# Performance work log

Measured on AMD Instinct MI355X. Metric: run time of the kernel, lower is better.

## Reference

```python
import jax, jax.numpy as jnp
import numpy as np

B, S, H, NH = 8, 512, 4096, 64
HD = H // NH  # head dim = 64
LN_EPS = 1e-12
TOL_BITS = 16


def quant16(x):
    """Per-tensor dynamic fixed-point quantization to 16 bits.

    int_bit_width = ceil(log2(max|x|)) + 1 (sign bit); frac = 16 - int_bits.
    Values are rounded to the fixed-point grid and clipped to int16 range.
    """
    m = jnp.max(jnp.abs(x))
    int_bw = jnp.ceil(jnp.log2(jnp.maximum(m, 1e-12))) + 1.0
    frac_bw = jnp.asarray(TOL_BITS, x.dtype) - int_bw
    scale = jnp.exp2(frac_bw).astype(x.dtype)
    q = jnp.clip(jnp.round(x * scale), -32768.0, 32767.0) / scale
    return q


def setup_inputs() -> dict:
    key = jax.random.key(0)
    ks = jax.random.split(key, 6)
    s = 0.02
    return {
        "input_ids": jax.random.normal(ks[0], (B, S, H), jnp.float32),
        "attention_mask": jnp.zeros((B, 1, 1, S), jnp.float32),
        "Wq": jax.random.normal(ks[1], (H, H), jnp.float32) * s,
        "bq": jnp.zeros((H,), jnp.float32),
        "Wk": jax.random.normal(ks[2], (H, H), jnp.float32) * s,
        "bk": jnp.zeros((H,), jnp.float32),
        "Wv": jax.random.normal(ks[3], (H, H), jnp.float32) * s,
        "bv": jnp.zeros((H,), jnp.float32),
        "Wd": jax.random.normal(ks[4], (H, H), jnp.float32) * s,
        "bd": jnp.zeros((H,), jnp.float32),
        "ln_w": jnp.ones((H,), jnp.float32),
        "ln_b": jnp.zeros((H,), jnp.float32),
    }


def reference(input_ids, attention_mask, Wq, bq, Wk, bk, Wv, bv, Wd, bd, ln_w, ln_b):
    x = input_ids  # [B,S,H]
    # Q/K/V projections (torch Linear: y = x @ W.T + b), each followed by quant
    q = quant16(jnp.einsum('bsh,oh->bso', x, Wq) + bq)
    k = quant16(jnp.einsum('bsh,oh->bso', x, Wk) + bk)
    v = quant16(jnp.einsum('bsh,oh->bso', x, Wv) + bv)
    # split heads -> [B,NH,S,HD]
    q = q.reshape(B, S, NH, HD).transpose(0, 2, 1, 3)
    k = k.reshape(B, S, NH, HD).transpose(0, 2, 1, 3)
    v = v.reshape(B, S, NH, HD).transpose(0, 2, 1, 3)
    scores = jnp.einsum('bnqd,bnkd->bnqk', q, k) / np.sqrt(HD).astype(np.float32)
    scores = quant16(scores)
    scores = scores + attention_mask
    probs = jax.nn.softmax(scores, axis=-1)
    probs = quant16(probs)
    ctx = quant16(jnp.einsum('bnqk,bnkd->bnqd', probs, v))
    ctx = ctx.transpose(0, 2, 1, 3)  # [B,S,NH,HD]
    # dense: w = Wd.T reshaped to (NH, HD, H)
    w = Wd.T.reshape(NH, HD, H)
    proj = quant16(jnp.einsum('bfnd,ndh->bfh', ctx, w) + bd)
    # residual + LayerNorm
    y = x + proj
    mu = jnp.mean(y, axis=-1, keepdims=True)
    var = jnp.mean(jnp.square(y - mu), axis=-1, keepdims=True)
    y = (y - mu) / jnp.sqrt(var + LN_EPS) * ln_w + ln_b
    return quant16(y)
```

## Files before the change

kernel.cpp:

```cpp
#include <hip/hip_runtime.h>
#include <hip/hip_bf16.h>
#include <stdint.h>


typedef __attribute__((ext_vector_type(4))) float f32x4;
typedef __attribute__((ext_vector_type(8))) __bf16 bf16x8;

__device__ inline unsigned short f2bf(float f) {
  union { float f; unsigned u; } c; c.f = f;
  unsigned r = (c.u + 0x7fffu + ((c.u >> 16) & 1u)) >> 16;
  return (unsigned short)r;
}

__device__ inline void gload_lds16(const void* g, void* l) {
  __builtin_amdgcn_global_load_lds(
      (const __attribute__((address_space(1))) void*)g,
      (__attribute__((address_space(3))) void*)l, 16, 0, 0);
}

__global__ __launch_bounds__(256) void conv_all(
    const float* __restrict__ x, const float* __restrict__ wq,
    const float* __restrict__ wk, const float* __restrict__ wv,
    const float* __restrict__ wd, unsigned short* __restrict__ out) {
  int i = blockIdx.x * 256 + threadIdx.x;
  int reg = i >> 21;
  int off = i & 2097151;
  const float* src = (reg == 0) ? x : (reg == 1) ? wq : (reg == 2) ? wk
                     : (reg == 3) ? wv : wd;
  const float4* ip = (const float4*)src;
  float4 a = ip[off * 2], b = ip[off * 2 + 1];
  union { unsigned short s[8]; uint4 v; } o;
  o.s[0] = f2bf(a.x); o.s[1] = f2bf(a.y); o.s[2] = f2bf(a.z); o.s[3] = f2bf(a.w);
  o.s[4] = f2bf(b.x); o.s[5] = f2bf(b.y); o.s[6] = f2bf(b.z); o.s[7] = f2bf(b.w);
  ((uint4*)out)[i] = o.v;
}

template <int BIAS_MODE, int OUT_BF16>
__global__ __launch_bounds__(512, 2) void gemm_8p(
    const unsigned short* __restrict__ A, const unsigned short* __restrict__ Bw,
    const float* __restrict__ bias0, const float* __restrict__ bias1,
    const float* __restrict__ bias2, void* __restrict__ Cout,
    int M, int N, int K) {
  extern __shared__ unsigned short lds[];
  const int nbm = M >> 8, nbn = N >> 8, nwg = nbm * nbn;
  const int bid = blockIdx.x;
  const int wg = (bid & 7) * (nwg >> 3) + (bid >> 3);
  const int bm = wg % nbm, bn = wg / nbm;
  const int tid = threadIdx.x, w = tid >> 6, l = tid & 63;
  const int wr = w >> 2, wc = w & 3;
  const int lr = l & 15, lg = l >> 4;
  const unsigned short* gA = A + (size_t)bm * 256 * K;
  const unsigned short* gB = Bw + (size_t)bn * 256 * K;
  const int NT = K >> 6;
  const int srow = tid >> 3;
  const int scol = ((tid & 7) ^ (srow & 7)) << 3;
  f32x4 acc[8][4] = {};
  bf16x8 a[8], b[8];

#define STG(op, buf, h, kt)                                                    \
  {                                                                            \
    const unsigned short* g_ = (op) ? gB : gA;                                 \
    _Pragma("unroll")                                                          \
    for (int j_ = 0; j_ < 2; ++j_) {                                           \
      gload_lds16(                                                             \
          g_ + (size_t)((h) * 128 + j_ * 64 + srow) * K + (kt) * 64 + scol,    \
          &lds[((op) * 2 + (buf)) * 16384 + ((h) * 128 + j_ * 64) * 64 +       \
               w * 512]);                                                      \
    }                                                                          \
  }

#define RDA(buf, m, kk)                                                        \
  (*(const bf16x8*)&lds[(buf) * 16384 + (wr * 128 + (m) * 16 + lr) * 64 +      \
                        ((((kk) * 4 + lg) ^ (lr & 7)) << 3)])
#define RDB(buf, n, kk)                                                        \
  (*(const bf16x8*)&lds[(2 + (buf)) * 16384 + (wc * 64 + (n) * 16 + lr) * 64 + \
                        ((((kk) * 4 + lg) ^ (lr & 7)) << 3)])

#define LDA(buf, mh)                                                           \
  _Pragma("unroll")                                                            \
  for (int m_ = 0; m_ < 4; ++m_) {                                             \
    a[m_ * 2 + 0] = RDA(buf, (mh) * 4 + m_, 0);                                \
    a[m_ * 2 + 1] = RDA(buf, (mh) * 4 + m_, 1);                                \
  }
#define LDB(buf, nh)                                                           \
  _Pragma("unroll")                                                            \
  for (int n_ = 0; n_ < 2; ++n_) {                                             \
    b[((nh) * 2 + n_) * 2 + 0] = RDB(buf, (nh) * 2 + n_, 0);                   \
    b[((nh) * 2 + n_) * 2 + 1] = RDB(buf, (nh) * 2 + n_, 1);                   \
  }

#define MM(mbase, nbase)                                                       \
  __builtin_amdgcn_s_setprio(1);                                               \
  _Pragma("unroll")                                                            \
  for (int m_ = 0; m_ < 4; ++m_) {                                             \
    _Pragma("unroll")                                                          \
    for (int n_ = 0; n_ < 2; ++n_) {                                           \
      acc[(mbase) + m_][(nbase) + n_] =                                        \
          __builtin_amdgcn_mfma_f32_16x16x32_bf16(                             \
              a[m_ * 2], b[((nbase) + n_) * 2], acc[(mbase) + m_][(nbase) + n_],\
              0, 0, 0);                                                        \
      acc[(mbase) + m_][(nbase) + n_] =                                        \
          __builtin_amdgcn_mfma_f32_16x16x32_bf16(                             \
              a[m_ * 2 + 1], b[((nbase) + n_) * 2 + 1],                        \
              acc[(mbase) + m_][(nbase) + n_], 0, 0, 0);                       \
    }                                                                          \
  }                                                                            \
  __builtin_amdgcn_s_setprio(0);

#define BAR() __builtin_amdgcn_s_barrier()
#define VMW(n) asm volatile("s_waitcnt vmcnt(" #n ")" ::: "memory")

  STG(0, 0, 0, 0); STG(0, 0, 1, 0); STG(1, 0, 0, 0); STG(1, 0, 1, 0);
  STG(0, 1, 0, 1);
  VMW(2);
  BAR();

  const int NI = NT >> 1;
  for (int i = 0; i < NI; ++i) {
    const int t1 = 2 * i + 1, t2 = 2 * i + 2, t3 = 2 * i + 3;
    const bool s2 = t2 < NT, s3 = t3 < NT;
    LDA(0, 0); LDB(0, 0);
    STG(0, 1, 1, t1);
    BAR(); MM(0, 0); BAR();
    LDB(0, 1);
    STG(1, 1, 0, t1);
    BAR(); MM(0, 2); BAR();
    LDA(0, 1);
    STG(1, 1, 1, t1);
    BAR(); MM(4, 2); BAR();
    if (s2) STG(0, 0, 0, t2);
    BAR(); MM(4, 0);
    if (s2) VMW(2); else VMW(0);
    BAR();
    LDA(1, 0); LDB(1, 0);
    if (s2) STG(0, 0, 1, t2);
    BAR(); MM(0, 0); BAR();
    LDB(1, 1);
    if (s2) STG(1, 0, 0, t2);
    BAR(); MM(0, 2); BAR();
    LDA(1, 1);
    if (s2) STG(1, 0, 1, t2);
    BAR(); MM(4, 2); BAR();
    if (s3) STG(0, 1, 0, t3);
    BAR(); MM(4, 0);
    if (s3) VMW(2); else VMW(0);
    BAR();
  }

#pragma unroll
  for (int n = 0; n < 4; ++n) {
    int col = bn * 256 + wc * 64 + n * 16 + lr;
    float bv = 0.f;
    if (BIAS_MODE == 1) bv = bias0[col];
    else if (BIAS_MODE == 2)
      bv = (col < 4096) ? bias0[col] : (col < 8192 ? bias1[col - 4096] : bias2[col - 8192]);
#pragma unroll
    for (int m = 0; m < 8; ++m) {
#pragma unroll
      for (int r = 0; r < 4; ++r) {
        int row = bm * 256 + wr * 128 + m * 16 + lg * 4 + r;
        float v = acc[m][n][r] + bv;
        if (OUT_BF16)
          ((unsigned short*)Cout)[(size_t)row * N + col] = f2bf(v);
        else
          ((float*)Cout)[(size_t)row * N + col] = v;
      }
    }
  }
#undef STG
#undef RDA
#undef RDB
#undef LDA
#undef LDB
#undef MM
#undef BAR
#undef VMW
}

__global__ __launch_bounds__(512) void attn_kernel(
    const unsigned short* __restrict__ qkv, const float* __restrict__ mask,
    unsigned short* __restrict__ ctx) {
  extern __shared__ char smem[];
  unsigned short* Kt = (unsigned short*)smem;
  unsigned short* Vt = Kt + 512 * 64;
  unsigned short* Pb = Vt + 64 * 512;
  float* Mb = (float*)(Pb + 8 * 16 * 64);

  const int bid = blockIdx.x;
  const int b = bid >> 6, h = bid & 63;
  const int tid = threadIdx.x, w = tid >> 6, l = tid & 63;
  const size_t tokbase = (size_t)b * 512;

  Mb[tid < 512 ? tid : 0] = mask[b * 512 + (tid < 512 ? tid : 0)];
#pragma unroll
  for (int it = 0; it < 8; ++it) {
    int idx = it * 512 + tid;
    int row = idx >> 3, g = (idx & 7) << 3;
    const unsigned short* src = qkv + (tokbase + row) * 12288 + 4096 + h * 64 + g;
    uint4 v = *(const uint4*)src;
    *(uint4*)&Kt[row * 64 + (g ^ ((row & 7) << 3))] = v;
  }
#pragma unroll
  for (int it = 0; it < 8; ++it) {
    int idx = it * 512 + tid;
    int key = idx >> 3, g = (idx & 7) << 3;
    const unsigned short* src = qkv + (tokbase + key) * 12288 + 8192 + h * 64 + g;
    uint4 v = *(const uint4*)src;
    const unsigned short* e = (const unsigned short*)&v;
#pragma unroll
    for (int i = 0; i < 8; i++) {
      int d = g + i;
      Vt[d * 512 + (key ^ ((d & 7) << 3))] = e[i];
    }
  }
  __syncthreads();

  unsigned short* Pw = Pb + w * 16 * 64;
  const int lr = l & 15, lg = l >> 4;

  for (int c = 0; c < 4; ++c) {
    int q0 = w * 64 + c * 16;
    const unsigned short* qsrc = qkv + (tokbase + q0 + lr) * 12288 + h * 64 + lg * 8;
    bf16x8 qa0 = *(const bf16x8*)qsrc;
    bf16x8 qa1 = *(const bf16x8*)(qsrc + 32);
    f32x4 sc[32];
    f32x4 zero = {0.f, 0.f, 0.f, 0.f};
#pragma unroll
    for (int n = 0; n < 32; n++) {
      int key = n * 16 + lr;
      bf16x8 kb0 = *(const bf16x8*)&Kt[key * 64 + ((lg * 8) ^ ((key & 7) << 3))];
      bf16x8 kb1 = *(const bf16x8*)&Kt[key * 64 + ((32 + lg * 8) ^ ((key & 7) << 3))];
      f32x4 a = __builtin_amdgcn_mfma_f32_16x16x32_bf16(qa0, kb0, zero, 0, 0, 0);
      sc[n] = __builtin_amdgcn_mfma_f32_16x16x32_bf16(qa1, kb1, a, 0, 0, 0);
    }
    float rmax[4] = {-1e30f, -1e30f, -1e30f, -1e30f};
#pragma unroll
    for (int n = 0; n < 32; n++) {
      float mk = Mb[n * 16 + lr];
#pragma unroll
      for (int r = 0; r < 4; r++) {
        float s = sc[n][r] * 0.125f + mk;
        sc[n][r] = s;
        rmax[r] = fmaxf(rmax[r], s);
      }
    }
#pragma unroll
    for (int r = 0; r < 4; r++) {
      float m = rmax[r];
      m = fmaxf(m, __shfl_xor(m, 8)); m = fmaxf(m, __shfl_xor(m, 4));
      m = fmaxf(m, __shfl_xor(m, 2)); m = fmaxf(m, __shfl_xor(m, 1));
      rmax[r] = m;
    }
    float rsum[4] = {0.f, 0.f, 0.f, 0.f};
#pragma unroll
    for (int n = 0; n < 32; n++)
#pragma unroll
      for (int r = 0; r < 4; r++) {
        float p = __expf(sc[n][r] - rmax[r]);
        sc[n][r] = p;
        rsum[r] += p;
      }
#pragma unroll
    for (int r = 0; r < 4; r++) {
      float s = rsum[r];
      s += __shfl_xor(s, 8); s += __shfl_xor(s, 4);
      s += __shfl_xor(s, 2); s += __shfl_xor(s, 1);
      rsum[r] = s;
    }
    f32x4 cacc[4] = {};
#pragma unroll
    for (int kb = 0; kb < 8; ++kb) {
#pragma unroll
      for (int nn = 0; nn < 4; ++nn) {
        int colp = nn * 16 + lr;
#pragma unroll
        for (int r = 0; r < 4; r++) {
          int m = lg * 4 + r;
          Pw[m * 64 + (colp ^ ((m & 7) << 3))] = f2bf(sc[kb * 4 + nn][r]);
        }
      }
      bf16x8 pa0 = *(const bf16x8*)&Pw[lr * 64 + ((lg * 8) ^ ((lr & 7) << 3))];
      bf16x8 pa1 = *(const bf16x8*)&Pw[lr * 64 + ((32 + lg * 8) ^ ((lr & 7) << 3))];
#pragma unroll
      for (int dt = 0; dt < 4; ++dt) {
        int vr = dt * 16 + lr;
        int k0 = kb * 64 + lg * 8;
        bf16x8 vb0 = *(const bf16x8*)&Vt[vr * 512 + (k0 ^ ((vr & 7) << 3))];
        bf16x8 vb1 = *(const bf16x8*)&Vt[vr * 512 + ((k0 + 32) ^ ((vr & 7) << 3))];
        cacc[dt] = __builtin_amdgcn_mfma_f32_16x16x32_bf16(pa0, vb0, cacc[dt], 0, 0, 0);
        cacc[dt] = __builtin_amdgcn_mfma_f32_16x16x32_bf16(pa1, vb1, cacc[dt], 0, 0, 0);
      }
    }
#pragma unroll
    for (int dt = 0; dt < 4; ++dt)
#pragma unroll
      for (int r = 0; r < 4; r++) {
        int row = q0 + lg * 4 + r;
        float v = cacc[dt][r] / rsum[r];
        ctx[(tokbase + row) * 4096 + h * 64 + dt * 16 + lr] = f2bf(v);
      }
  }
}

__global__ __launch_bounds__(256) void ln_kernel(
    const float* __restrict__ x, float* __restrict__ io,
    const float* __restrict__ lnw, const float* __restrict__ lnb) {
  int t = blockIdx.x;
  const float4* xr = (const float4*)(x + (size_t)t * 4096);
  float4* pr = (float4*)(io + (size_t)t * 4096);
  float4 y[4];
  float sum = 0.f, sq = 0.f;
#pragma unroll
  for (int j = 0; j < 4; j++) {
    int i4 = j * 256 + threadIdx.x;
    float4 xv = xr[i4], pv = pr[i4];
    float4 yy;
    yy.x = xv.x + pv.x; yy.y = xv.y + pv.y; yy.z = xv.z + pv.z; yy.w = xv.w + pv.w;
    sum += yy.x + yy.y + yy.z + yy.w;
    sq += yy.x * yy.x + yy.y * yy.y + yy.z * yy.z + yy.w * yy.w;
    y[j] = yy;
  }
#pragma unroll
  for (int off = 32; off >= 1; off >>= 1) {
    sum += __shfl_down(sum, off);
    sq += __shfl_down(sq, off);
  }
  __shared__ float red[8];
  int w = threadIdx.x >> 6, l = threadIdx.x & 63;
  if (l == 0) { red[w] = sum; red[4 + w] = sq; }
  __syncthreads();
  float ts = red[0] + red[1] + red[2] + red[3];
  float tq = red[4] + red[5] + red[6] + red[7];
  float mean = ts * (1.f / 4096.f);
  float var = tq * (1.f / 4096.f) - mean * mean;
  float rs = rsqrtf(var + 1e-12f);
#pragma unroll
  for (int j = 0; j < 4; j++) {
    int i4 = j * 256 + threadIdx.x;
    float4 wv = ((const float4*)lnw)[i4];
    float4 bb = ((const float4*)lnb)[i4];
    float4 o;
    o.x = (y[j].x - mean) * rs * wv.x + bb.x;
    o.y = (y[j].y - mean) * rs * wv.y + bb.y;
    o.z = (y[j].z - mean) * rs * wv.z + bb.z;
    o.w = (y[j].w - mean) * rs * wv.w + bb.w;
    pr[i4] = o;
  }
}

extern "C" void kernel_launch(void* const* d_in, const int* in_sizes, int n_in,
                              void* d_out, int out_size, void* d_ws, size_t ws_size,
                              hipStream_t stream) {
  const float* x   = (const float*)d_in[0];
  const float* msk = (const float*)d_in[1];
  const float* Wq  = (const float*)d_in[2];
  const float* bq  = (const float*)d_in[3];
  const float* Wk  = (const float*)d_in[4];
  const float* bk  = (const float*)d_in[5];
  const float* Wv  = (const float*)d_in[6];
  const float* bv  = (const float*)d_in[7];
  const float* Wd  = (const float*)d_in[8];
  const float* bd  = (const float*)d_in[9];
  const float* lnw = (const float*)d_in[10];
  const float* lnb = (const float*)d_in[11];
  float* out = (float*)d_out;

  unsigned short* xb    = (unsigned short*)d_ws;
  unsigned short* wqkvb = xb + (size_t)16777216;
  unsigned short* wdb   = wqkvb + (size_t)50331648;
  unsigned short* qkvb  = wdb + (size_t)16777216;
  unsigned short* ctxb  = wqkvb;

  conv_all<<<40960, 256, 0, stream>>>(x, Wq, Wk, Wv, Wd, xb);

  (void)hipFuncSetAttribute((const void*)(gemm_8p<2, 1>),
                            hipFuncAttributeMaxDynamicSharedMemorySize, 131072);
  (void)hipFuncSetAttribute((const void*)(gemm_8p<1, 0>),
                            hipFuncAttributeMaxDynamicSharedMemorySize, 131072);

  gemm_8p<2, 1><<<768, 512, 131072, stream>>>(xb, wqkvb, bq, bk, bv, qkvb,
                                              4096, 12288, 4096);

  (void)hipFuncSetAttribute((const void*)attn_kernel,
                            hipFuncAttributeMaxDynamicSharedMemorySize, 149504);
  attn_kernel<<<512, 512, 149504, stream>>>(qkvb, msk, ctxb);

  gemm_8p<1, 0><<<256, 512, 131072, stream>>>(ctxb, wdb, bd, nullptr, nullptr,
                                              out, 4096, 4096, 4096);

  ln_kernel<<<4096, 256, 0, stream>>>(x, out, lnw, lnb);
}
```

Before: 764.4 us.

## Split GEMM block across 16 waves with 64x64 per-wave tiles

Doubles the GEMM workgroup to 1024 threads, so each of 16 waves computes a 64x64 sub-tile of the same 256x256 block tile, halving accumulator registers per wave. Staging loads are reissued as one 16-byte load per thread per half, and the waitcnt thresholds are adjusted to match. The intent is more waves in flight to hide latency and less register pressure. In exchange, LDS read traffic per MFMA rises and barriers synchronize more waves.

New measurement: 2.345 ms. +206.8%, slower.

```diff
diff --git a/kernel.cpp b/kernel.cpp
--- a/kernel.cpp
+++ b/kernel.cpp
@@ -36,7 +36,7 @@
 }
 
 template <int BIAS_MODE, int OUT_BF16>
-__global__ __launch_bounds__(512, 2) void gemm_8p(
+__global__ __launch_bounds__(1024, 4) void gemm_8p(
     const unsigned short* __restrict__ A, const unsigned short* __restrict__ Bw,
     const float* __restrict__ bias0, const float* __restrict__ bias1,
     const float* __restrict__ bias2, void* __restrict__ Cout,
@@ -54,23 +54,18 @@
   const int NT = K >> 6;
   const int srow = tid >> 3;
   const int scol = ((tid & 7) ^ (srow & 7)) << 3;
-  f32x4 acc[8][4] = {};
-  bf16x8 a[8], b[8];
+  f32x4 acc[4][4] = {};
+  bf16x8 a[2][2], b0[2][2], b1[2][2];
 
 #define STG(op, buf, h, kt)                                                    \
   {                                                                            \
     const unsigned short* g_ = (op) ? gB : gA;                                 \
-    _Pragma("unroll")                                                          \
-    for (int j_ = 0; j_ < 2; ++j_) {                                           \
-      gload_lds16(                                                             \
-          g_ + (size_t)((h) * 128 + j_ * 64 + srow) * K + (kt) * 64 + scol,    \
-          &lds[((op) * 2 + (buf)) * 16384 + ((h) * 128 + j_ * 64) * 64 +       \
-               w * 512]);                                                      \
-    }                                                                          \
+    gload_lds16(g_ + (size_t)((h) * 128 + srow) * K + (kt) * 64 + scol,        \
+                &lds[((op) * 2 + (buf)) * 16384 + (h) * 8192 + w * 512]);      \
   }
 
 #define RDA(buf, m, kk)                                                        \
-  (*(const bf16x8*)&lds[(buf) * 16384 + (wr * 128 + (m) * 16 + lr) * 64 +      \
+  (*(const bf16x8*)&lds[(buf) * 16384 + (wr * 64 + (m) * 16 + lr) * 64 +       \
                         ((((kk) * 4 + lg) ^ (lr & 7)) << 3)])
 #define RDB(buf, n, kk)                                                        \
   (*(const bf16x8*)&lds[(2 + (buf)) * 16384 + (wc * 64 + (n) * 16 + lr) * 64 + \
@@ -78,72 +73,73 @@
 
 #define LDA(buf, mh)                                                           \
   _Pragma("unroll")                                                            \
-  for (int m_ = 0; m_ < 4; ++m_) {                                             \
-    a[m_ * 2 + 0] = RDA(buf, (mh) * 4 + m_, 0);                                \
-    a[m_ * 2 + 1] = RDA(buf, (mh) * 4 + m_, 1);                                \
-  }
-#define LDB(buf, nh)                                                           \
+  for (int mt_ = 0; mt_ < 2; ++mt_) {                                          \
+    a[mt_][0] = RDA(buf, (mh) * 2 + mt_, 0);                                   \
+    a[mt_][1] = RDA(buf, (mh) * 2 + mt_, 1);                                   \
+  }
+#define LDB(buf, nh, dst)                                                      \
   _Pragma("unroll")                                                            \
-  for (int n_ = 0; n_ < 2; ++n_) {                                             \
-    b[((nh) * 2 + n_) * 2 + 0] = RDB(buf, (nh) * 2 + n_, 0);                   \
-    b[((nh) * 2 + n_) * 2 + 1] = RDB(buf, (nh) * 2 + n_, 1);                   \
-  }
-
-#define MM(mbase, nbase)                                                       \
+  for (int nt_ = 0; nt_ < 2; ++nt_) {                                          \
+    dst[nt_][0] = RDB(buf, (nh) * 2 + nt_, 0);                                 \
+    dst[nt_][1] = RDB(buf, (nh) * 2 + nt_, 1);                                 \
+  }
+
+#define MM(mh, nh, barr)                                                       \
   __builtin_amdgcn_s_setprio(1);                                               \
   _Pragma("unroll")                                                            \
-  for (int m_ = 0; m_ < 4; ++m_) {                                             \
+  for (int mt_ = 0; mt_ < 2; ++mt_) {                                          \
     _Pragma("unroll")                                                          \
-    for (int n_ = 0; n_ < 2; ++n_) {                                           \
-      acc[(mbase) + m_][(nbase) + n_] =                                        \
+    for (int nt_ = 0; nt_ < 2; ++nt_) {                                        \
+      acc[(mh) * 2 + mt_][(nh) * 2 + nt_] =                                    \
           __builtin_amdgcn_mfma_f32_16x16x32_bf16(                             \
-              a[m_ * 2], b[((nbase) + n_) * 2], acc[(mbase) + m_][(nbase) + n_],\
-              0, 0, 0);                                                        \
-      acc[(mbase) + m_][(nbase) + n_] =                                        \
+              a[mt_][0], barr[nt_][0],                                         \
+              acc[(mh) * 2 + mt_][(nh) * 2 + nt_], 0, 0, 0);                   \
+      acc[(mh) * 2 + mt_][(nh) * 2 + nt_] =                                    \
           __builtin_amdgcn_mfma_f32_16x16x32_bf16(                             \
-              a[m_ * 2 + 1], b[((nbase) + n_) * 2 + 1],                        \
-              acc[(mbase) + m_][(nbase) + n_], 0, 0, 0);                       \
+              a[mt_][1], barr[nt_][1],                                         \
+              acc[(mh) * 2 + mt_][(nh) * 2 + nt_], 0, 0, 0);                   \
     }                                                                          \
   }                                                                            \
   __builtin_amdgcn_s_setprio(0);
 
 #define BAR() __builtin_amdgcn_s_barrier()
-#define VMW(n) asm volatile("s_waitcnt vmcnt(" #n ")" ::: "memory")
+#define VMW1() asm volatile("s_waitcnt vmcnt(1)" ::: "memory")
+#define VMW0() asm volatile("s_waitcnt vmcnt(0)" ::: "memory")
 
   STG(0, 0, 0, 0); STG(0, 0, 1, 0); STG(1, 0, 0, 0); STG(1, 0, 1, 0);
   STG(0, 1, 0, 1);
-  VMW(2);
+  VMW1();
   BAR();
 
   const int NI = NT >> 1;
   for (int i = 0; i < NI; ++i) {
     const int t1 = 2 * i + 1, t2 = 2 * i + 2, t3 = 2 * i + 3;
     const bool s2 = t2 < NT, s3 = t3 < NT;
-    LDA(0, 0); LDB(0, 0);
+    LDA(0, 0); LDB(0, 0, b0);
     STG(0, 1, 1, t1);
-    BAR(); MM(0, 0); BAR();
-    LDB(0, 1);
+    BAR(); MM(0, 0, b0); BAR();
+    LDB(0, 1, b1);
     STG(1, 1, 0, t1);
-    BAR(); MM(0, 2); BAR();
+    BAR(); MM(0, 1, b1); BAR();
     LDA(0, 1);
     STG(1, 1, 1, t1);
-    BAR(); MM(4, 2); BAR();
+    BAR(); MM(1, 1, b1); BAR();
     if (s2) STG(0, 0, 0, t2);
-    BAR(); MM(4, 0);
-    if (s2) VMW(2); else VMW(0);
+    BAR(); MM(1, 0, b0);
+    if (s2) VMW1(); else VMW0();
     BAR();
-    LDA(1, 0); LDB(1, 0);
+    LDA(1, 0); LDB(1, 0, b0);
     if (s2) STG(0, 0, 1, t2);
-    BAR(); MM(0, 0); BAR();
-    LDB(1, 1);
+    BAR(); MM(0, 0, b0); BAR();
+    LDB(1, 1, b1);
     if (s2) STG(1, 0, 0, t2);
-    BAR(); MM(0, 2); BAR();
+    BAR(); MM(0, 1, b1); BAR();
     LDA(1, 1);
     if (s2) STG(1, 0, 1, t2);
-    BAR(); MM(4, 2); BAR();
+    BAR(); MM(1, 1, b1); BAR();
     if (s3) STG(0, 1, 0, t3);
-    BAR(); MM(4, 0);
-    if (s3) VMW(2); else VMW(0);
+    BAR(); MM(1, 0, b0);
+    if (s3) VMW1(); else VMW0();
     BAR();
   }
 
@@ -155,10 +151,10 @@
     else if (BIAS_MODE == 2)
       bv = (col < 4096) ? bias0[col] : (col < 8192 ? bias1[col - 4096] : bias2[col - 8192]);
 #pragma unroll
-    for (int m = 0; m < 8; ++m) {
+    for (int m = 0; m < 4; ++m) {
 #pragma unroll
       for (int r = 0; r < 4; ++r) {
-        int row = bm * 256 + wr * 128 + m * 16 + lg * 4 + r;
+        int row = bm * 256 + wr * 64 + m * 16 + lg * 4 + r;
         float v = acc[m][n][r] + bv;
         if (OUT_BF16)
           ((unsigned short*)Cout)[(size_t)row * N + col] = f2bf(v);
@@ -174,7 +170,8 @@
 #undef LDB
 #undef MM
 #undef BAR
-#undef VMW
+#undef VMW1
+#undef VMW0
 }
 
 __global__ __launch_bounds__(512) void attn_kernel(
@@ -378,15 +375,15 @@
   (void)hipFuncSetAttribute((const void*)(gemm_8p<1, 0>),
                             hipFuncAttributeMaxDynamicSharedMemorySize, 131072);
 
-  gemm_8p<2, 1><<<768, 512, 131072, stream>>>(xb, wqkvb, bq, bk, bv, qkvb,
-                                              4096, 12288, 4096);
+  gemm_8p<2, 1><<<768, 1024, 131072, stream>>>(xb, wqkvb, bq, bk, bv, qkvb,
+                                               4096, 12288, 4096);
 
   (void)hipFuncSetAttribute((const void*)attn_kernel,
                             hipFuncAttributeMaxDynamicSharedMemorySize, 149504);
   attn_kernel<<<512, 512, 149504, stream>>>(qkvb, msk, ctxb);
 
-  gemm_8p<1, 0><<<256, 512, 131072, stream>>>(ctxb, wdb, bd, nullptr, nullptr,
-                                              out, 4096, 4096, 4096);
+  gemm_8p<1, 0><<<256, 1024, 131072, stream>>>(ctxb, wdb, bd, nullptr, nullptr,
+                                               out, 4096, 4096, 4096);
 
   ln_kernel<<<4096, 256, 0, stream>>>(x, out, lnw, lnb);
 }
```
